# Optimization experiments

Measured on AMD Instinct MI355X. Metric: run time of the kernel, lower is better.

The kernel has to match this reference:

```python
import jax, jax.numpy as jnp
import numpy as np

N_NODES = 4096
N_EDGES = 131072
NUM_USERS = 50000
NUM_ITEMS = 50000
EMB = 64
NUM_CLASSES = 41476
BN_EPS = 1e-5


def _seg_sum(x, idx, n):
    return jax.ops.segment_sum(x, idx, num_segments=n)


def gcn_conv(x, ei, W, b):
    # PyG GCNConv: linear, add self-loops, sym norm D^-1/2 (A+I) D^-1/2, sum-agg, +bias
    n = x.shape[0]
    h = x @ W
    loop = jnp.arange(n, dtype=ei.dtype)
    row = jnp.concatenate([ei[0], loop])
    col = jnp.concatenate([ei[1], loop])
    deg = _seg_sum(jnp.ones_like(col, h.dtype), col, n)
    dinv = jnp.where(deg > 0, deg ** -0.5, 0.0)
    norm = dinv[row] * dinv[col]
    return _seg_sum(h[row] * norm[:, None], col, n) + b


def sage_conv(x, ei, Wl, bl, Wr):
    # PyG SAGEConv (mean aggr): mean_neighbors(x) @ Wl + bl + x @ Wr
    n = x.shape[0]
    ones = jnp.ones((ei.shape[1],), x.dtype)
    cnt = _seg_sum(ones, ei[1], n)
    agg = _seg_sum(x[ei[0]], ei[1], n) / jnp.maximum(cnt, 1.0)[:, None]
    return agg @ Wl + bl + x @ Wr


def cheb_conv(x, ei, W0, W1, b):
    # PyG ChebConv K=2, sym norm, lambda_max=2: L_hat = L - I = -D^-1/2 A D^-1/2
    # out = x @ W0 + (L_hat x) @ W1 + b
    n = x.shape[0]
    ones = jnp.ones((ei.shape[1],), x.dtype)
    deg = _seg_sum(ones, ei[0], n)  # row-sum degree (get_laplacian)
    dinv = jnp.where(deg > 0, deg ** -0.5, 0.0)
    w = -(dinv[ei[0]] * dinv[ei[1]])
    tx1 = _seg_sum(x[ei[0]] * w[:, None], ei[1], n)
    return x @ W0 + tx1 @ W1 + b


def gat_conv(x, ei, W, a_src, a_dst, b):
    # PyG GATConv heads=1, concat=False, self-loops added, leaky_relu(0.2) + softmax over in-edges
    n = x.shape[0]
    h = x @ W
    loop = jnp.arange(n, dtype=ei.dtype)
    row = jnp.concatenate([ei[0], loop])
    col = jnp.concatenate([ei[1], loop])
    a_s = h @ a_src  # [n]
    a_d = h @ a_dst
    e = jax.nn.leaky_relu(a_s[row] + a_d[col], 0.2)
    emax = jax.ops.segment_max(e, col, num_segments=n)  # every segment nonempty (self-loops)
    ex = jnp.exp(e - emax[col])
    denom = _seg_sum(ex, col, n)
    alpha = ex / denom[col]
    return _seg_sum(h[row] * alpha[:, None], col, n) + b


def batch_norm(x, g, be):
    mu = jnp.mean(x, axis=0)
    var = jnp.var(x, axis=0)
    return (x - mu) * jax.lax.rsqrt(var + BN_EPS) * g + be


def setup_inputs() -> dict:
    key = jax.random.key(0)
    ks = iter(jax.random.split(key, 48))
    nrm = lambda shape, s=0.05: jax.random.normal(next(ks), shape, jnp.float32) * s
    edge_index = jax.random.randint(next(ks), (2, N_EDGES), 0, N_NODES, jnp.int32)
    node_x = jax.random.randint(next(ks), (N_NODES, 2), 0, NUM_USERS, jnp.int32)
    inp = dict(
        edge_index=edge_index, node_x=node_x,
        user_emb_w=nrm((NUM_USERS, EMB)), item_emb_w=nrm((NUM_ITEMS, EMB)),
        mlp_w1=nrm((2 * EMB, 1024)), mlp_b1=jnp.zeros((1024,), jnp.float32),
        mlp_w2=nrm((1024, 512)), mlp_b2=jnp.zeros((512,), jnp.float32),
        gcn_w1=nrm((512, 256)), gcn_b1=jnp.zeros((256,), jnp.float32),
        bn1_g=jnp.ones((256,), jnp.float32), bn1_b=jnp.zeros((256,), jnp.float32),
        gcn_w2=nrm((256, 128)), gcn_b2=jnp.zeros((128,), jnp.float32),
        bn2_g=jnp.ones((128,), jnp.float32), bn2_b=jnp.zeros((128,), jnp.float32),
        sage_wl=nrm((128, 128)), sage_bl=jnp.zeros((128,), jnp.float32), sage_wr=nrm((128, 128)),
        cheb_w0=nrm((128, 128)), cheb_w1=nrm((128, 128)), cheb_b=jnp.zeros((128,), jnp.float32),
        gat1_w=nrm((128, 128)), gat1_asrc=nrm((128,)), gat1_adst=nrm((128,)), gat1_b=jnp.zeros((128,), jnp.float32),
        gat2_w=nrm((128, 128)), gat2_asrc=nrm((128,)), gat2_adst=nrm((128,)), gat2_b=jnp.zeros((128,), jnp.float32),
        pred_w=nrm((128, NUM_CLASSES)), pred_b=jnp.zeros((NUM_CLASSES,), jnp.float32),
    )
    return inp


def reference(edge_index, node_x, user_emb_w, item_emb_w, mlp_w1, mlp_b1, mlp_w2, mlp_b2,
              gcn_w1, gcn_b1, bn1_g, bn1_b, gcn_w2, gcn_b2, bn2_g, bn2_b,
              sage_wl, sage_bl, sage_wr, cheb_w0, cheb_w1, cheb_b,
              gat1_w, gat1_asrc, gat1_adst, gat1_b, gat2_w, gat2_asrc, gat2_adst, gat2_b,
              pred_w, pred_b):
    u = user_emb_w[node_x[:, 0]]
    i = item_emb_w[node_x[:, 1]]
    x = jnp.concatenate([u, i], axis=1)  # [N, 2*EMB]
    x = jax.nn.relu(x @ mlp_w1 + mlp_b1)  # dropout = identity (eval mode)
    x = jax.nn.relu(x @ mlp_w2 + mlp_b2)
    x = jax.nn.relu(batch_norm(gcn_conv(x, edge_index, gcn_w1, gcn_b1), bn1_g, bn1_b))
    x = jax.nn.relu(batch_norm(gcn_conv(x, edge_index, gcn_w2, gcn_b2), bn2_g, bn2_b))
    x = jax.nn.relu(sage_conv(x, edge_index, sage_wl, sage_bl, sage_wr))
    x = jax.nn.relu(cheb_conv(x, edge_index, cheb_w0, cheb_w1, cheb_b))
    x = jax.nn.elu(gat_conv(x, edge_index, gat1_w, gat1_asrc, gat1_adst, gat1_b))
    x = jax.nn.elu(gat_conv(x, edge_index, gat2_w, gat2_asrc, gat2_adst, gat2_b))
    return x @ pred_w + pred_b  # [N, NUM_CLASSES]
```

## Files before the change

kernel.cpp:

```cpp
#include <hip/hip_runtime.h>
#include <math.h>

#define NN 4096
#define NE 131072
#define NCLS 41476
#define NPAD 41600

typedef __attribute__((ext_vector_type(8))) unsigned short ushort8;
typedef __attribute__((ext_vector_type(8))) __bf16 bf16x8;
typedef __attribute__((ext_vector_type(4))) float f32x4;

__device__ __forceinline__ unsigned short f2bf(float f) {
  unsigned u = __float_as_uint(f);
  unsigned r = u + 0x7fffu + ((u >> 16) & 1u);
  return (unsigned short)(r >> 16);
}
__device__ __forceinline__ float bf2f(unsigned short u) {
  return __uint_as_float(((unsigned)u) << 16);
}

__global__ void k_gather(const int* __restrict__ node_x, const float* __restrict__ uw,
                         const float* __restrict__ iw, unsigned short* __restrict__ x0) {
  int n = blockIdx.x, t = threadIdx.x;
  int u = node_x[n * 2], it = node_x[n * 2 + 1];
  float v = (t < 64) ? uw[u * 64 + t] : iw[it * 64 + (t - 64)];
  x0[n * 128 + t] = f2bf(v);
}

struct CvtDesc { const float* src; unsigned short* dst; int K, N, ld, koff, tile0, ntx; };
struct CvtArgs { CvtDesc d[11]; };

__global__ void k_cvt_all(CvtArgs a) {
  __shared__ float s[32][33];
  int b = blockIdx.x;
  int di = 0;
#pragma unroll
  for (int i = 1; i < 11; i++)
    if (a.d[i].tile0 <= b) di = i;
  const CvtDesc dd = a.d[di];
  int t = b - dd.tile0;
  int n0 = (t % dd.ntx) * 32, k0 = (t / dd.ntx) * 32;
  int tt = threadIdx.x, c = tt & 31, r8 = tt >> 5;
#pragma unroll
  for (int r = 0; r < 4; r++) {
    int k = k0 + r8 + r * 8, n = n0 + c;
    s[r8 + r * 8][c] = (n < dd.N) ? dd.src[(size_t)k * dd.N + n] : 0.f;
  }
  __syncthreads();
#pragma unroll
  for (int r = 0; r < 4; r++) {
    int n = n0 + r8 + r * 8, k = k0 + c;
    dd.dst[(size_t)n * dd.ld + dd.koff + k] = f2bf(s[c][r8 + r * 8]);
  }
}

template <int OUTBF>
__global__ __launch_bounds__(256) void k_bgemm(const unsigned short* __restrict__ A,
                                               const unsigned short* __restrict__ Bt,
                                               const float* __restrict__ bias,
                                               void* __restrict__ Cv, int N, int K, int relu) {
  __shared__ unsigned short As[128 * 128];
  __shared__ unsigned short Bs[128 * 128];
  int m0 = blockIdx.y * 128;
  int n0 = blockIdx.x * 128;
  int tid = threadIdx.x;
  int wave = tid >> 6, lane = tid & 63;
  int wm = (wave >> 1) * 64, wn = (wave & 1) * 64;
  int lr = lane & 15, lg = lane >> 4;
  f32x4 acc[4][4] = {};
  for (int k0 = 0; k0 < K; k0 += 128) {
#pragma unroll
    for (int i = 0; i < 8; i++) {
      int idx = tid + i * 256;
      int row = idx >> 4, ku = idx & 15;
      int sw = (ku ^ (row & 7)) * 8;
      *reinterpret_cast<ushort8*>(As + row * 128 + sw) =
          *reinterpret_cast<const ushort8*>(A + (size_t)(m0 + row) * K + k0 + ku * 8);
      *reinterpret_cast<ushort8*>(Bs + row * 128 + sw) =
          *reinterpret_cast<const ushort8*>(Bt + (size_t)(n0 + row) * K + k0 + ku * 8);
    }
    __syncthreads();
#pragma unroll
    for (int kk = 0; kk < 4; kk++) {
      bf16x8 af[4], bfr[4];
#pragma unroll
      for (int mi = 0; mi < 4; mi++) {
        int row = wm + mi * 16 + lr;
        af[mi] = __builtin_bit_cast(
            bf16x8, *reinterpret_cast<const ushort8*>(As + row * 128 + (((kk * 4 + lg) ^ (row & 7)) * 8)));
        int col = wn + mi * 16 + lr;
        bfr[mi] = __builtin_bit_cast(
            bf16x8, *reinterpret_cast<const ushort8*>(Bs + col * 128 + (((kk * 4 + lg) ^ (col & 7)) * 8)));
      }
#pragma unroll
      for (int mi = 0; mi < 4; mi++)
#pragma unroll
        for (int ni = 0; ni < 4; ni++)
          acc[mi][ni] = __builtin_amdgcn_mfma_f32_16x16x32_bf16(af[mi], bfr[ni], acc[mi][ni], 0, 0, 0);
    }
    __syncthreads();
  }
#pragma unroll
  for (int mi = 0; mi < 4; mi++) {
#pragma unroll
    for (int ni = 0; ni < 4; ni++) {
      int col = n0 + wn + ni * 16 + lr;
      if (col < N) {
        float bv = bias ? bias[col] : 0.f;
#pragma unroll
        for (int r = 0; r < 4; r++) {
          int row = m0 + wm + mi * 16 + lg * 4 + r;
          float v = acc[mi][ni][r] + bv;
          if (relu) v = fmaxf(v, 0.f);
          if (OUTBF)
            ((unsigned short*)Cv)[(size_t)row * N + col] = f2bf(v);
          else
            ((float*)Cv)[(size_t)row * N + col] = v;
        }
      }
    }
  }
}

__global__ __launch_bounds__(256) void k_bgemm_s(const unsigned short* __restrict__ A,
                                                 const unsigned short* __restrict__ Bt,
                                                 const float* __restrict__ bias,
                                                 unsigned short* __restrict__ C, int ldC,
                                                 int K, int relu) {
  __shared__ unsigned short As[32 * 64];
  __shared__ unsigned short Bs[128 * 64];
  int m0 = blockIdx.y * 32;
  int n0 = blockIdx.x * 128;
  int tid = threadIdx.x;
  int wave = tid >> 6, lane = tid & 63;
  int wn = wave * 32;
  int lr = lane & 15, lg = lane >> 4;
  f32x4 acc[2][2] = {};
  for (int k0 = 0; k0 < K; k0 += 64) {
    {
      int row = tid >> 3, u = tid & 7, sw = (u ^ (row & 7)) * 8;
      *reinterpret_cast<ushort8*>(As + row * 64 + sw) =
          *reinterpret_cast<const ushort8*>(A + (size_t)(m0 + row) * K + k0 + u * 8);
    }
#pragma unroll
    for (int i = 0; i < 4; i++) {
      int idx = tid + i * 256;
      int row = idx >> 3, u = idx & 7, sw = (u ^ (row & 7)) * 8;
      *reinterpret_cast<ushort8*>(Bs + row * 64 + sw) =
          *reinterpret_cast<const ushort8*>(Bt + (size_t)(n0 + row) * K + k0 + u * 8);
    }
    __syncthreads();
#pragma unroll
    for (int kk = 0; kk < 2; kk++) {
      bf16x8 af[2], bfr[2];
#pragma unroll
      for (int mi = 0; mi < 2; mi++) {
        int row = mi * 16 + lr;
        af[mi] = __builtin_bit_cast(
            bf16x8, *reinterpret_cast<const ushort8*>(As + row * 64 + (((kk * 4 + lg) ^ (row & 7)) * 8)));
        int col = wn + mi * 16 + lr;
        bfr[mi] = __builtin_bit_cast(
            bf16x8, *reinterpret_cast<const ushort8*>(Bs + col * 64 + (((kk * 4 + lg) ^ (col & 7)) * 8)));
      }
#pragma unroll
      for (int mi = 0; mi < 2; mi++)
#pragma unroll
        for (int ni = 0; ni < 2; ni++)
          acc[mi][ni] = __builtin_amdgcn_mfma_f32_16x16x32_bf16(af[mi], bfr[ni], acc[mi][ni], 0, 0, 0);
    }
    __syncthreads();
  }
#pragma unroll
  for (int mi = 0; mi < 2; mi++) {
#pragma unroll
    for (int ni = 0; ni < 2; ni++) {
      int col = n0 + wn + ni * 16 + lr;
      float bv = bias ? bias[col] : 0.f;
#pragma unroll
      for (int r = 0; r < 4; r++) {
        int row = m0 + mi * 16 + lg * 4 + r;
        float v = acc[mi][ni][r] + bv;
        if (relu) v = fmaxf(v, 0.f);
        C[(size_t)row * ldC + col] = f2bf(v);
      }
    }
  }
}

__global__ void k_count2(const int* __restrict__ ei, int* __restrict__ deg0,
                         int* __restrict__ deg1) {
  for (int i = blockIdx.x * blockDim.x + threadIdx.x; i < 2 * NE; i += gridDim.x * blockDim.x) {
    int v = ei[i];
    atomicAdd((i < NE ? deg0 : deg1) + v, 1);
  }
}

__global__ void k_dinv(const int* __restrict__ deg, float* __restrict__ dinv, int n, int self) {
  int i = blockIdx.x * blockDim.x + threadIdx.x;
  if (i < n) {
    int d = deg[i] + self;
    dinv[i] = d > 0 ? rsqrtf((float)d) : 0.f;
  }
}

__global__ void k_scan4096(const int* __restrict__ deg, int* __restrict__ rowptr,
                           int* __restrict__ cursor, float* __restrict__ dinvA) {
  __shared__ int s[1024];
  int t = threadIdx.x;
  int4 d = *reinterpret_cast<const int4*>(deg + t * 4);
  float4 dv;
  dv.x = rsqrtf((float)(d.x + 1));
  dv.y = rsqrtf((float)(d.y + 1));
  dv.z = rsqrtf((float)(d.z + 1));
  dv.w = rsqrtf((float)(d.w + 1));
  *reinterpret_cast<float4*>(dinvA + t * 4) = dv;
  int sum = d.x + d.y + d.z + d.w;
  s[t] = sum;
  __syncthreads();
  for (int off = 1; off < 1024; off <<= 1) {
    int x = (t >= off) ? s[t - off] : 0;
    __syncthreads();
    s[t] += x;
    __syncthreads();
  }
  int base = s[t] - sum;
  int4 o;
  o.x = base; o.y = base + d.x; o.z = o.y + d.y; o.w = o.z + d.z;
  *reinterpret_cast<int4*>(rowptr + t * 4) = o;
  *reinterpret_cast<int4*>(cursor + t * 4) = o;
  if (t == 1023) rowptr[4096] = base + sum;
}

__global__ void k_fill(const int* __restrict__ ei0, const int* __restrict__ ei1,
                       int* __restrict__ cursor, int* __restrict__ csr_src) {
  int e = blockIdx.x * blockDim.x + threadIdx.x;
  if (e < NE) {
    int pos = atomicAdd(&cursor[ei1[e]], 1);
    csr_src[pos] = ei0[e];
  }
}

template <int LOGF>
__global__ void k_gcn_agg(const unsigned short* __restrict__ h, const int* __restrict__ rowptr,
                          const int* __restrict__ csr_src, const float* __restrict__ dinv,
                          float* __restrict__ out) {
  __shared__ int sld[128];
  __shared__ float wld[128];
  int c = blockIdx.x, f = threadIdx.x;
  float dc = dinv[c];
  int r0 = rowptr[c], r1 = rowptr[c + 1];
  float acc = bf2f(h[((size_t)c << LOGF) + f]) * dc;
  for (int base = r0; base < r1; base += 128) {
    int nb = min(128, r1 - base);
    if (f < nb) {
      int s = csr_src[base + f];
      sld[f] = s;
      wld[f] = dinv[s];
    }
    __syncthreads();
    for (int i = 0; i < nb; i++) acc += bf2f(h[((size_t)sld[i] << LOGF) + f]) * wld[i];
    __syncthreads();
  }
  out[((size_t)c << LOGF) + f] = acc * dc;
}

__global__ void k_sage_agg(const unsigned short* __restrict__ x, const int* __restrict__ rowptr,
                           const int* __restrict__ csr_src, unsigned short* __restrict__ out) {
  __shared__ int sld[128];
  int c = blockIdx.x, f = threadIdx.x;
  int r0 = rowptr[c], r1 = rowptr[c + 1];
  float acc = 0.f;
  for (int base = r0; base < r1; base += 128) {
    int nb = min(128, r1 - base);
    if (f < nb) sld[f] = csr_src[base + f];
    __syncthreads();
    for (int i = 0; i < nb; i++) acc += bf2f(x[(size_t)sld[i] * 256 + f]);
    __syncthreads();
  }
  out[(size_t)c * 256 + f] = f2bf(acc / fmaxf((float)(r1 - r0), 1.f));
}

__global__ void k_cheb_agg(const unsigned short* __restrict__ x, const int* __restrict__ rowptr,
                           const int* __restrict__ csr_src, const float* __restrict__ dinv0,
                           unsigned short* __restrict__ out) {
  __shared__ int sld[128];
  __shared__ float wld[128];
  int c = blockIdx.x, f = threadIdx.x;
  int r0 = rowptr[c], r1 = rowptr[c + 1];
  float acc = 0.f;
  for (int base = r0; base < r1; base += 128) {
    int nb = min(128, r1 - base);
    if (f < nb) {
      int s = csr_src[base + f];
      sld[f] = s;
      wld[f] = dinv0[s];
    }
    __syncthreads();
    for (int i = 0; i < nb; i++) acc += bf2f(x[(size_t)sld[i] * 256 + f]) * wld[i];
    __syncthreads();
  }
  out[(size_t)c * 256 + f] = f2bf(-acc * dinv0[c]);
}

__global__ void k_gat_agg(const unsigned short* __restrict__ h, const int* __restrict__ rowptr,
                          const int* __restrict__ csr_src, const float* __restrict__ a_s,
                          const float* __restrict__ a_d, const float* __restrict__ bias,
                          unsigned short* __restrict__ out) {
  __shared__ int sld[128];
  __shared__ float eld[128];
  int c = blockIdx.x, f = threadIdx.x;
  int r0 = rowptr[c], r1 = rowptr[c + 1];
  float adc = a_d[c];
  float es = a_s[c] + adc;
  es = es >= 0.f ? es : 0.2f * es;
  float m = es;
  for (int base = r0; base < r1; base += 128) {
    int nb = min(128, r1 - base);
    if (f < nb) {
      float v = a_s[csr_src[base + f]] + adc;
      eld[f] = v >= 0.f ? v : 0.2f * v;
    }
    __syncthreads();
    for (int i = 0; i < nb; i++) m = fmaxf(m, eld[i]);
    __syncthreads();
  }
  float den = expf(es - m);
  float acc = den * bf2f(h[((size_t)c << 7) + f]);
  for (int base = r0; base < r1; base += 128) {
    int nb = min(128, r1 - base);
    if (f < nb) {
      int s = csr_src[base + f];
      sld[f] = s;
      float v = a_s[s] + adc;
      v = v >= 0.f ? v : 0.2f * v;
      eld[f] = expf(v - m);
    }
    __syncthreads();
    for (int i = 0; i < nb; i++) {
      float w = eld[i];
      acc += w * bf2f(h[((size_t)sld[i] << 7) + f]);
      den += w;
    }
    __syncthreads();
  }
  float v = acc / den + bias[f];
  out[((size_t)c << 7) + f] = f2bf(v > 0.f ? v : expm1f(v));
}

__global__ void k_bn_stats(const float* __restrict__ x, float* __restrict__ psum,
                           float* __restrict__ psq, int F) {
  int tid = threadIdx.x;
  int f = tid & (F - 1);
  int rstep = 256 / F;
  int r0 = tid / F;
  int base = blockIdx.x * 64;
  float s = 0.f, s2 = 0.f;
  for (int rr = r0; rr < 64; rr += rstep) {
    float v = x[(size_t)(base + rr) * F + f];
    s += v;
    s2 += v * v;
  }
  int slot = blockIdx.x * rstep + r0;
  psum[(size_t)slot * F + f] = s;
  psq[(size_t)slot * F + f] = s2;
}

__global__ void k_bn_final(const float* __restrict__ psum, const float* __restrict__ psq,
                           const float* __restrict__ g, const float* __restrict__ be,
                           float* __restrict__ scale, float* __restrict__ shift, int F) {
  int f = threadIdx.x;
  int S = 16384 / F;
  float s = 0.f, s2 = 0.f;
  for (int i = 0; i < S; i++) {
    s += psum[(size_t)i * F + f];
    s2 += psq[(size_t)i * F + f];
  }
  float invM = 1.f / (float)NN;
  float mu = s * invM;
  float var = s2 * invM - mu * mu;
  float sc = g[f] * rsqrtf(var + 1e-5f);
  scale[f] = sc;
  shift[f] = be[f] - mu * sc;
}

__global__ void k_bn_apply(const float* __restrict__ x, const float* __restrict__ scale,
                           const float* __restrict__ shift, unsigned short* __restrict__ y,
                           int ldY, int logF, int n) {
  int F1 = (1 << logF) - 1;
  for (int i = blockIdx.x * blockDim.x + threadIdx.x; i < n; i += gridDim.x * blockDim.x) {
    int row = i >> logF, f = i & F1;
    float v = fmaxf(x[i] * scale[f] + shift[f], 0.f);
    y[(size_t)row * ldY + f] = f2bf(v);
  }
}

__global__ void k_gat_dots(const unsigned short* __restrict__ h, const float* __restrict__ asrc,
                           const float* __restrict__ adst, float* __restrict__ a_s,
                           float* __restrict__ a_d) {
  int n = blockIdx.x * 4 + (threadIdx.x >> 6), l = threadIdx.x & 63;
  float h0 = bf2f(h[n * 128 + l]), h1 = bf2f(h[n * 128 + 64 + l]);
  float hs = h0 * asrc[l] + h1 * asrc[64 + l];
  float hd = h0 * adst[l] + h1 * adst[64 + l];
  for (int off = 32; off; off >>= 1) {
    hs += __shfl_down(hs, off, 64);
    hd += __shfl_down(hd, off, 64);
  }
  if (l == 0) {
    a_s[n] = hs;
    a_d[n] = hd;
  }
}

static inline int cdiv(int a, int b) { return (a + b - 1) / b; }

extern "C" void kernel_launch(void* const* d_in, const int* in_sizes, int n_in,
                              void* d_out, int out_size, void* d_ws, size_t ws_size,
                              hipStream_t stream) {
  const int* ei = (const int*)d_in[0];
  const int* ei0 = ei;
  const int* ei1 = ei + NE;
  const int* node_x = (const int*)d_in[1];
  const float* user_w = (const float*)d_in[2];
  const float* item_w = (const float*)d_in[3];
  const float* mlp_w1 = (const float*)d_in[4];
  const float* mlp_b1 = (const float*)d_in[5];
  const float* mlp_w2 = (const float*)d_in[6];
  const float* mlp_b2 = (const float*)d_in[7];
  const float* gcn_w1 = (const float*)d_in[8];
  const float* bn1_g = (const float*)d_in[10];
  const float* bn1_b = (const float*)d_in[11];
  const float* gcn_w2 = (const float*)d_in[12];
  const float* bn2_g = (const float*)d_in[14];
  const float* bn2_b = (const float*)d_in[15];
  const float* sage_wl = (const float*)d_in[16];
  const float* sage_bl = (const float*)d_in[17];
  const float* sage_wr = (const float*)d_in[18];
  const float* cheb_w0 = (const float*)d_in[19];
  const float* cheb_w1 = (const float*)d_in[20];
  const float* cheb_b = (const float*)d_in[21];
  const float* gat1_w = (const float*)d_in[22];
  const float* gat1_as = (const float*)d_in[23];
  const float* gat1_ad = (const float*)d_in[24];
  const float* gat1_b = (const float*)d_in[25];
  const float* gat2_w = (const float*)d_in[26];
  const float* gat2_as = (const float*)d_in[27];
  const float* gat2_ad = (const float*)d_in[28];
  const float* gat2_b = (const float*)d_in[29];
  const float* pred_w = (const float*)d_in[30];
  const float* pred_b = (const float*)d_in[31];

  char* w = (char*)d_ws;
  size_t off = 0;
  auto alloc = [&](size_t bytes) -> char* {
    char* p = w + off;
    off = (off + bytes + 255) & ~(size_t)255;
    return p;
  };
  unsigned short* x0b = (unsigned short*)alloc((size_t)NN * 128 * 2);
  unsigned short* x1b = (unsigned short*)alloc((size_t)NN * 1024 * 2);
  unsigned short* x2b = (unsigned short*)alloc((size_t)NN * 512 * 2);
  unsigned short* h1b = (unsigned short*)alloc((size_t)NN * 256 * 2);
  unsigned short* xab = (unsigned short*)alloc((size_t)NN * 256 * 2);
  unsigned short* catS = (unsigned short*)alloc((size_t)NN * 256 * 2);
  unsigned short* catC = (unsigned short*)alloc((size_t)NN * 256 * 2);
  unsigned short* xb2 = (unsigned short*)alloc((size_t)NN * 128 * 2);
  unsigned short* hb = (unsigned short*)alloc((size_t)NN * 128 * 2);
  unsigned short* xa2 = (unsigned short*)alloc((size_t)NN * 128 * 2);
  unsigned short* xb3 = (unsigned short*)alloc((size_t)NN * 128 * 2);
  float* agg = (float*)alloc((size_t)NN * 256 * 4);
  unsigned short* w1t = (unsigned short*)alloc((size_t)1024 * 128 * 2);
  unsigned short* w2t = (unsigned short*)alloc((size_t)512 * 1024 * 2);
  unsigned short* g1t = (unsigned short*)alloc((size_t)256 * 512 * 2);
  unsigned short* g2t = (unsigned short*)alloc((size_t)128 * 256 * 2);
  unsigned short* sgt = (unsigned short*)alloc((size_t)128 * 256 * 2);
  unsigned short* cht = (unsigned short*)alloc((size_t)128 * 256 * 2);
  unsigned short* a1t = (unsigned short*)alloc((size_t)128 * 128 * 2);
  unsigned short* a2t = (unsigned short*)alloc((size_t)128 * 128 * 2);
  unsigned short* predT = (unsigned short*)alloc((size_t)NPAD * 128 * 2);
  int* deg0 = (int*)alloc(NN * 4);
  int* deg1 = (int*)alloc(NN * 4);
  int* rowptr = (int*)alloc((NN + 1) * 4);
  int* cursor = (int*)alloc(NN * 4);
  int* csr_src = (int*)alloc(NE * 4);
  float* dinvA = (float*)alloc(NN * 4);
  float* dinv0 = (float*)alloc(NN * 4);
  float* a_s = (float*)alloc(NN * 4);
  float* a_d = (float*)alloc(NN * 4);
  float* psum = (float*)alloc(16384 * 4);
  float* psq = (float*)alloc(16384 * 4);
  float* bscale = (float*)alloc(256 * 4);
  float* bshift = (float*)alloc(256 * 4);

  CvtArgs ca;
  int t0 = 0;
  auto mkd = [&](int i, const float* src, unsigned short* dst, int K, int N, int ld, int koff,
                 int ntx) {
    ca.d[i] = {src, dst, K, N, ld, koff, t0, ntx};
    t0 += ntx * (K / 32);
  };
  mkd(0, mlp_w1, w1t, 128, 1024, 128, 0, 32);
  mkd(1, mlp_w2, w2t, 1024, 512, 1024, 0, 16);
  mkd(2, gcn_w1, g1t, 512, 256, 512, 0, 8);
  mkd(3, gcn_w2, g2t, 256, 128, 256, 0, 4);
  mkd(4, sage_wl, sgt, 128, 128, 256, 0, 4);
  mkd(5, sage_wr, sgt, 128, 128, 256, 128, 4);
  mkd(6, cheb_w0, cht, 128, 128, 256, 0, 4);
  mkd(7, cheb_w1, cht, 128, 128, 256, 128, 4);
  mkd(8, gat1_w, a1t, 128, 128, 128, 0, 4);
  mkd(9, gat2_w, a2t, 128, 128, 128, 0, 4);
  mkd(10, pred_w, predT, 128, NCLS, 128, 0, NPAD / 32);
  k_cvt_all<<<t0, 256, 0, stream>>>(ca);

  hipMemsetAsync(deg0, 0, 2 * NN * 4, stream);
  k_count2<<<512, 256, 0, stream>>>(ei, deg0, deg1);
  k_scan4096<<<1, 1024, 0, stream>>>(deg1, rowptr, cursor, dinvA);
  k_fill<<<cdiv(NE, 256), 256, 0, stream>>>(ei0, ei1, cursor, csr_src);
  k_dinv<<<cdiv(NN, 256), 256, 0, stream>>>(deg0, dinv0, NN, 0);

  k_gather<<<NN, 128, 0, stream>>>(node_x, user_w, item_w, x0b);
  k_bgemm<1><<<dim3(8, 32), 256, 0, stream>>>(x0b, w1t, mlp_b1, x1b, 1024, 128, 1);
  k_bgemm<1><<<dim3(4, 32), 256, 0, stream>>>(x1b, w2t, mlp_b2, x2b, 512, 1024, 1);

  k_bgemm_s<<<dim3(2, 128), 256, 0, stream>>>(x2b, g1t, nullptr, h1b, 256, 512, 0);
  k_gcn_agg<8><<<NN, 256, 0, stream>>>(h1b, rowptr, csr_src, dinvA, agg);
  k_bn_stats<<<64, 256, 0, stream>>>(agg, psum, psq, 256);
  k_bn_final<<<1, 256, 0, stream>>>(psum, psq, bn1_g, bn1_b, bscale, bshift, 256);
  k_bn_apply<<<1024, 256, 0, stream>>>(agg, bscale, bshift, xab, 256, 8, NN * 256);

  k_bgemm_s<<<dim3(1, 128), 256, 0, stream>>>(xab, g2t, nullptr, hb, 128, 256, 0);
  k_gcn_agg<7><<<NN, 128, 0, stream>>>(hb, rowptr, csr_src, dinvA, agg);
  k_bn_stats<<<64, 256, 0, stream>>>(agg, psum, psq, 128);
  k_bn_final<<<1, 128, 0, stream>>>(psum, psq, bn2_g, bn2_b, bscale, bshift, 128);
  k_bn_apply<<<1024, 256, 0, stream>>>(agg, bscale, bshift, catS + 128, 256, 7, NN * 128);

  k_sage_agg<<<NN, 128, 0, stream>>>(catS + 128, rowptr, csr_src, catS);
  k_bgemm_s<<<dim3(1, 128), 256, 0, stream>>>(catS, sgt, sage_bl, catC, 256, 256, 1);

  k_cheb_agg<<<NN, 128, 0, stream>>>(catC, rowptr, csr_src, dinv0, catC + 128);
  k_bgemm_s<<<dim3(1, 128), 256, 0, stream>>>(catC, cht, cheb_b, xb2, 128, 256, 1);

  k_bgemm_s<<<dim3(1, 128), 256, 0, stream>>>(xb2, a1t, nullptr, hb, 128, 128, 0);
  k_gat_dots<<<NN / 4, 256, 0, stream>>>(hb, gat1_as, gat1_ad, a_s, a_d);
  k_gat_agg<<<NN, 128, 0, stream>>>(hb, rowptr, csr_src, a_s, a_d, gat1_b, xa2);

  k_bgemm_s<<<dim3(1, 128), 256, 0, stream>>>(xa2, a2t, nullptr, hb, 128, 128, 0);
  k_gat_dots<<<NN / 4, 256, 0, stream>>>(hb, gat2_as, gat2_ad, a_s, a_d);
  k_gat_agg<<<NN, 128, 0, stream>>>(hb, rowptr, csr_src, a_s, a_d, gat2_b, xb3);

  k_bgemm<0><<<dim3(NPAD / 128, 32), 256, 0, stream>>>(xb3, predT, pred_b, (float*)d_out, NCLS, 128, 0);
}
```

Baseline: 510.0 us.

## Fuse BN-apply and GAT dots into GEMMs, stage GEMM epilogue via LDS, widen aggregation

```diff
diff --git a/kernel.cpp b/kernel.cpp
--- a/kernel.cpp
+++ b/kernel.cpp
@@ -59,8 +59,10 @@
                                                const unsigned short* __restrict__ Bt,
                                                const float* __restrict__ bias,
                                                void* __restrict__ Cv, int N, int K, int relu) {
-  __shared__ unsigned short As[128 * 128];
-  __shared__ unsigned short Bs[128 * 128];
+  __shared__ union SU {
+    struct { unsigned short As[128 * 128]; unsigned short Bs[128 * 128]; } s;
+    float Ls[128 * 132];
+  } u;
   int m0 = blockIdx.y * 128;
   int n0 = blockIdx.x * 128;
   int tid = threadIdx.x;
@@ -74,9 +76,9 @@
       int idx = tid + i * 256;
       int row = idx >> 4, ku = idx & 15;
       int sw = (ku ^ (row & 7)) * 8;
-      *reinterpret_cast<ushort8*>(As + row * 128 + sw) =
+      *reinterpret_cast<ushort8*>(u.s.As + row * 128 + sw) =
           *reinterpret_cast<const ushort8*>(A + (size_t)(m0 + row) * K + k0 + ku * 8);
-      *reinterpret_cast<ushort8*>(Bs + row * 128 + sw) =
+      *reinterpret_cast<ushort8*>(u.s.Bs + row * 128 + sw) =
           *reinterpret_cast<const ushort8*>(Bt + (size_t)(n0 + row) * K + k0 + ku * 8);
     }
     __syncthreads();
@@ -87,10 +89,10 @@
       for (int mi = 0; mi < 4; mi++) {
         int row = wm + mi * 16 + lr;
         af[mi] = __builtin_bit_cast(
-            bf16x8, *reinterpret_cast<const ushort8*>(As + row * 128 + (((kk * 4 + lg) ^ (row & 7)) * 8)));
+            bf16x8, *reinterpret_cast<const ushort8*>(u.s.As + row * 128 + (((kk * 4 + lg) ^ (row & 7)) * 8)));
         int col = wn + mi * 16 + lr;
         bfr[mi] = __builtin_bit_cast(
-            bf16x8, *reinterpret_cast<const ushort8*>(Bs + col * 128 + (((kk * 4 + lg) ^ (col & 7)) * 8)));
+            bf16x8, *reinterpret_cast<const ushort8*>(u.s.Bs + col * 128 + (((kk * 4 + lg) ^ (col & 7)) * 8)));
       }
 #pragma unroll
       for (int mi = 0; mi < 4; mi++)
@@ -101,53 +103,109 @@
     __syncthreads();
   }
 #pragma unroll
-  for (int mi = 0; mi < 4; mi++) {
+  for (int mi = 0; mi < 4; mi++)
 #pragma unroll
     for (int ni = 0; ni < 4; ni++) {
-      int col = n0 + wn + ni * 16 + lr;
-      if (col < N) {
-        float bv = bias ? bias[col] : 0.f;
-#pragma unroll
-        for (int r = 0; r < 4; r++) {
-          int row = m0 + wm + mi * 16 + lg * 4 + r;
-          float v = acc[mi][ni][r] + bv;
-          if (relu) v = fmaxf(v, 0.f);
-          if (OUTBF)
-            ((unsigned short*)Cv)[(size_t)row * N + col] = f2bf(v);
-          else
-            ((float*)Cv)[(size_t)row * N + col] = v;
-        }
-      }
-    }
-  }
-}
-
-__global__ __launch_bounds__(256) void k_bgemm_s(const unsigned short* __restrict__ A,
+      int cl = wn + ni * 16 + lr;
+#pragma unroll
+      for (int r = 0; r < 4; r++) {
+        int rl = wm + mi * 16 + lg * 4 + r;
+        u.Ls[rl * 132 + cl] = acc[mi][ni][r];
+      }
+    }
+  __syncthreads();
+  float* Cf = (float*)Cv;
+  unsigned short* Cb = (unsigned short*)Cv;
+#pragma unroll
+  for (int it = 0; it < 8; it++) {
+    int idx = tid + it * 256;
+    int rl = idx >> 4, cb = (idx & 15) * 8;
+    float vv[8];
+    *reinterpret_cast<float4*>(&vv[0]) = *reinterpret_cast<float4*>(&u.Ls[rl * 132 + cb]);
+    *reinterpret_cast<float4*>(&vv[4]) = *reinterpret_cast<float4*>(&u.Ls[rl * 132 + cb + 4]);
+    int col = n0 + cb;
+    size_t row = m0 + rl;
+    if (OUTBF) {
+      float4 b0 = *reinterpret_cast<const float4*>(bias + col);
+      float4 b1 = *reinterpret_cast<const float4*>(bias + col + 4);
+      float bb[8] = {b0.x, b0.y, b0.z, b0.w, b1.x, b1.y, b1.z, b1.w};
+      ushort8 ov;
+#pragma unroll
+      for (int j = 0; j < 8; j++) {
+        float v = vv[j] + bb[j];
+        if (relu) v = fmaxf(v, 0.f);
+        ov[j] = f2bf(v);
+      }
+      *reinterpret_cast<ushort8*>(Cb + row * N + col) = ov;
+    } else {
+      if (col + 8 <= N) {
+        float4 b0 = *reinterpret_cast<const float4*>(bias + col);
+        float4 b1 = *reinterpret_cast<const float4*>(bias + col + 4);
+        float4 o0 = {vv[0] + b0.x, vv[1] + b0.y, vv[2] + b0.z, vv[3] + b0.w};
+        float4 o1 = {vv[4] + b1.x, vv[5] + b1.y, vv[6] + b1.z, vv[7] + b1.w};
+        *reinterpret_cast<float4*>(Cf + row * N + col) = o0;
+        *reinterpret_cast<float4*>(Cf + row * N + col + 4) = o1;
+      } else {
+#pragma unroll
+        for (int j = 0; j < 8; j++)
+          if (col + j < N) Cf[row * N + col + j] = vv[j] + bias[col + j];
+      }
+    }
+  }
+}
+
+template <int MODE>
+__global__ __launch_bounds__(256) void k_bgemm_s(const void* __restrict__ Av,
                                                  const unsigned short* __restrict__ Bt,
                                                  const float* __restrict__ bias,
                                                  unsigned short* __restrict__ C, int ldC,
-                                                 int K, int relu) {
+                                                 int K, int relu,
+                                                 const float* __restrict__ scale,
+                                                 const float* __restrict__ shift,
+                                                 const float* __restrict__ asrc,
+                                                 const float* __restrict__ adst,
+                                                 float* __restrict__ o_as,
+                                                 float* __restrict__ o_ad) {
   __shared__ unsigned short As[32 * 64];
   __shared__ unsigned short Bs[128 * 64];
+  __shared__ float sc[256], sh[256];
+  __shared__ float sas[4][32], sad[4][32];
   int m0 = blockIdx.y * 32;
   int n0 = blockIdx.x * 128;
   int tid = threadIdx.x;
   int wave = tid >> 6, lane = tid & 63;
   int wn = wave * 32;
   int lr = lane & 15, lg = lane >> 4;
+  if (MODE == 1) {
+    if (tid < K) { sc[tid] = scale[tid]; sh[tid] = shift[tid]; }
+    __syncthreads();
+  }
   f32x4 acc[2][2] = {};
   for (int k0 = 0; k0 < K; k0 += 64) {
     {
-      int row = tid >> 3, u = tid & 7, sw = (u ^ (row & 7)) * 8;
-      *reinterpret_cast<ushort8*>(As + row * 64 + sw) =
-          *reinterpret_cast<const ushort8*>(A + (size_t)(m0 + row) * K + k0 + u * 8);
+      int row = tid >> 3, uu = tid & 7, sw = (uu ^ (row & 7)) * 8;
+      if (MODE == 1) {
+        const float* Af = (const float*)Av;
+        const float* p = Af + (size_t)(m0 + row) * K + k0 + uu * 8;
+        float4 p0 = *reinterpret_cast<const float4*>(p);
+        float4 p1 = *reinterpret_cast<const float4*>(p + 4);
+        int kb = k0 + uu * 8;
+        float pv[8] = {p0.x, p0.y, p0.z, p0.w, p1.x, p1.y, p1.z, p1.w};
+        ushort8 o;
+#pragma unroll
+        for (int j = 0; j < 8; j++) o[j] = f2bf(fmaxf(pv[j] * sc[kb + j] + sh[kb + j], 0.f));
+        *reinterpret_cast<ushort8*>(As + row * 64 + sw) = o;
+      } else {
+        *reinterpret_cast<ushort8*>(As + row * 64 + sw) =
+            *reinterpret_cast<const ushort8*>((const unsigned short*)Av + (size_t)(m0 + row) * K + k0 + uu * 8);
+      }
     }
 #pragma unroll
     for (int i = 0; i < 4; i++) {
       int idx = tid + i * 256;
-      int row = idx >> 3, u = idx & 7, sw = (u ^ (row & 7)) * 8;
+      int row = idx >> 3, uu = idx & 7, sw = (uu ^ (row & 7)) * 8;
       *reinterpret_cast<ushort8*>(Bs + row * 64 + sw) =
-          *reinterpret_cast<const ushort8*>(Bt + (size_t)(n0 + row) * K + k0 + u * 8);
+          *reinterpret_cast<const ushort8*>(Bt + (size_t)(n0 + row) * K + k0 + uu * 8);
     }
     __syncthreads();
 #pragma unroll
@@ -170,19 +228,47 @@
     }
     __syncthreads();
   }
+  float dss[2][4] = {}, dsd[2][4] = {};
 #pragma unroll
   for (int mi = 0; mi < 2; mi++) {
 #pragma unroll
     for (int ni = 0; ni < 2; ni++) {
       int col = n0 + wn + ni * 16 + lr;
       float bv = bias ? bias[col] : 0.f;
+      float ac = (MODE == 2) ? asrc[col] : 0.f;
+      float dc = (MODE == 2) ? adst[col] : 0.f;
 #pragma unroll
       for (int r = 0; r < 4; r++) {
         int row = m0 + mi * 16 + lg * 4 + r;
         float v = acc[mi][ni][r] + bv;
         if (relu) v = fmaxf(v, 0.f);
         C[(size_t)row * ldC + col] = f2bf(v);
-      }
+        if (MODE == 2) { dss[mi][r] += v * ac; dsd[mi][r] += v * dc; }
+      }
+    }
+  }
+  if (MODE == 2) {
+#pragma unroll
+    for (int mi = 0; mi < 2; mi++)
+#pragma unroll
+      for (int r = 0; r < 4; r++) {
+#pragma unroll
+        for (int mask = 1; mask < 16; mask <<= 1) {
+          dss[mi][r] += __shfl_xor(dss[mi][r], mask);
+          dsd[mi][r] += __shfl_xor(dsd[mi][r], mask);
+        }
+        if (lr == 0) {
+          int rowloc = mi * 16 + lg * 4 + r;
+          sas[wave][rowloc] = dss[mi][r];
+          sad[wave][rowloc] = dsd[mi][r];
+        }
+      }
+    __syncthreads();
+    if (tid < 32) {
+      float s = sas[0][tid] + sas[1][tid] + sas[2][tid] + sas[3][tid];
+      float d = sad[0][tid] + sad[1][tid] + sad[2][tid] + sad[3][tid];
+      o_as[m0 + tid] = s;
+      o_ad[m0 + tid] = d;
     }
   }
 }
@@ -195,25 +281,19 @@
   }
 }
 
-__global__ void k_dinv(const int* __restrict__ deg, float* __restrict__ dinv, int n, int self) {
-  int i = blockIdx.x * blockDim.x + threadIdx.x;
-  if (i < n) {
-    int d = deg[i] + self;
-    dinv[i] = d > 0 ? rsqrtf((float)d) : 0.f;
-  }
-}
-
-__global__ void k_scan4096(const int* __restrict__ deg, int* __restrict__ rowptr,
-                           int* __restrict__ cursor, float* __restrict__ dinvA) {
+__global__ void k_scan4096(const int* __restrict__ deg1, const int* __restrict__ deg0,
+                           int* __restrict__ rowptr, int* __restrict__ cursor,
+                           float* __restrict__ dinvA, float* __restrict__ dinv0) {
   __shared__ int s[1024];
   int t = threadIdx.x;
-  int4 d = *reinterpret_cast<const int4*>(deg + t * 4);
-  float4 dv;
-  dv.x = rsqrtf((float)(d.x + 1));
-  dv.y = rsqrtf((float)(d.y + 1));
-  dv.z = rsqrtf((float)(d.z + 1));
-  dv.w = rsqrtf((float)(d.w + 1));
+  int4 d = *reinterpret_cast<const int4*>(deg1 + t * 4);
+  float4 dv = {rsqrtf((float)(d.x + 1)), rsqrtf((float)(d.y + 1)),
+               rsqrtf((float)(d.z + 1)), rsqrtf((float)(d.w + 1))};
   *reinterpret_cast<float4*>(dinvA + t * 4) = dv;
+  int4 d0 = *reinterpret_cast<const int4*>(deg0 + t * 4);
+  float4 dv0 = {d0.x > 0 ? rsqrtf((float)d0.x) : 0.f, d0.y > 0 ? rsqrtf((float)d0.y) : 0.f,
+                d0.z > 0 ? rsqrtf((float)d0.z) : 0.f, d0.w > 0 ? rsqrtf((float)d0.w) : 0.f};
+  *reinterpret_cast<float4*>(dinv0 + t * 4) = dv0;
   int sum = d.x + d.y + d.z + d.w;
   s[t] = sum;
   __syncthreads();
@@ -240,44 +320,78 @@
   }
 }
 
-template <int LOGF>
+template <int VEC>
 __global__ void k_gcn_agg(const unsigned short* __restrict__ h, const int* __restrict__ rowptr,
                           const int* __restrict__ csr_src, const float* __restrict__ dinv,
                           float* __restrict__ out) {
+  constexpr int F = 64 * VEC;
   __shared__ int sld[128];
   __shared__ float wld[128];
-  int c = blockIdx.x, f = threadIdx.x;
+  __shared__ float red[3][64 * VEC];
+  int c = blockIdx.x, tid = threadIdx.x, wv = tid >> 6, ln = tid & 63;
   float dc = dinv[c];
   int r0 = rowptr[c], r1 = rowptr[c + 1];
-  float acc = bf2f(h[((size_t)c << LOGF) + f]) * dc;
+  float acc[VEC] = {};
   for (int base = r0; base < r1; base += 128) {
     int nb = min(128, r1 - base);
-    if (f < nb) {
-      int s = csr_src[base + f];
-      sld[f] = s;
-      wld[f] = dinv[s];
-    }
-    __syncthreads();
-    for (int i = 0; i < nb; i++) acc += bf2f(h[((size_t)sld[i] << LOGF) + f]) * wld[i];
-    __syncthreads();
-  }
-  out[((size_t)c << LOGF) + f] = acc * dc;
+    __syncthreads();
+    if (tid < nb) { int s = csr_src[base + tid]; sld[tid] = s; wld[tid] = dinv[s]; }
+    __syncthreads();
+    for (int i = wv; i < nb; i += 4) {
+      float w = wld[i];
+      const unsigned short* p = h + (size_t)sld[i] * F + ln * VEC;
+      if (VEC == 2) {
+        ushort2 v = *reinterpret_cast<const ushort2*>(p);
+        acc[0] += bf2f(v.x) * w; acc[1] += bf2f(v.y) * w;
+      } else {
+        ushort4 v = *reinterpret_cast<const ushort4*>(p);
+        acc[0] += bf2f(v.x) * w; acc[1] += bf2f(v.y) * w;
+        acc[2] += bf2f(v.z) * w; acc[3] += bf2f(v.w) * w;
+      }
+    }
+  }
+  if (wv) {
+#pragma unroll
+    for (int j = 0; j < VEC; j++) red[wv - 1][ln * VEC + j] = acc[j];
+  }
+  __syncthreads();
+  if (wv == 0) {
+    const unsigned short* pc = h + (size_t)c * F + ln * VEC;
+#pragma unroll
+    for (int j = 0; j < VEC; j++) {
+      acc[j] += red[0][ln * VEC + j] + red[1][ln * VEC + j] + red[2][ln * VEC + j];
+      acc[j] += bf2f(pc[j]) * dc;
+      out[(size_t)c * F + ln * VEC + j] = acc[j] * dc;
+    }
+  }
 }
 
 __global__ void k_sage_agg(const unsigned short* __restrict__ x, const int* __restrict__ rowptr,
                            const int* __restrict__ csr_src, unsigned short* __restrict__ out) {
   __shared__ int sld[128];
-  int c = blockIdx.x, f = threadIdx.x;
+  __shared__ float red[3][128];
+  int c = blockIdx.x, tid = threadIdx.x, wv = tid >> 6, ln = tid & 63;
   int r0 = rowptr[c], r1 = rowptr[c + 1];
-  float acc = 0.f;
+  float a0 = 0.f, a1 = 0.f;
   for (int base = r0; base < r1; base += 128) {
     int nb = min(128, r1 - base);
-    if (f < nb) sld[f] = csr_src[base + f];
-    __syncthreads();
-    for (int i = 0; i < nb; i++) acc += bf2f(x[(size_t)sld[i] * 256 + f]);
-    __syncthreads();
-  }
-  out[(size_t)c * 256 + f] = f2bf(acc / fmaxf((float)(r1 - r0), 1.f));
+    __syncthreads();
+    if (tid < nb) sld[tid] = csr_src[base + tid];
+    __syncthreads();
+    for (int i = wv; i < nb; i += 4) {
+      ushort2 v = *reinterpret_cast<const ushort2*>(x + (size_t)sld[i] * 256 + ln * 2);
+      a0 += bf2f(v.x); a1 += bf2f(v.y);
+    }
+  }
+  if (wv) { red[wv - 1][ln * 2] = a0; red[wv - 1][ln * 2 + 1] = a1; }
+  __syncthreads();
+  if (wv == 0) {
+    a0 += red[0][ln * 2] + red[1][ln * 2] + red[2][ln * 2];
+    a1 += red[0][ln * 2 + 1] + red[1][ln * 2 + 1] + red[2][ln * 2 + 1];
+    float inv = 1.f / fmaxf((float)(r1 - r0), 1.f);
+    ushort2 o; o.x = f2bf(a0 * inv); o.y = f2bf(a1 * inv);
+    *reinterpret_cast<ushort2*>(out + (size_t)c * 256 + ln * 2) = o;
+  }
 }
 
 __global__ void k_cheb_agg(const unsigned short* __restrict__ x, const int* __restrict__ rowptr,
@@ -285,21 +399,30 @@
                            unsigned short* __restrict__ out) {
   __shared__ int sld[128];
   __shared__ float wld[128];
-  int c = blockIdx.x, f = threadIdx.x;
+  __shared__ float red[3][128];
+  int c = blockIdx.x, tid = threadIdx.x, wv = tid >> 6, ln = tid & 63;
   int r0 = rowptr[c], r1 = rowptr[c + 1];
-  float acc = 0.f;
+  float a0 = 0.f, a1 = 0.f;
   for (int base = r0; base < r1; base += 128) {
     int nb = min(128, r1 - base);
-    if (f < nb) {
-      int s = csr_src[base + f];
-      sld[f] = s;
-      wld[f] = dinv0[s];
-    }
-    __syncthreads();
-    for (int i = 0; i < nb; i++) acc += bf2f(x[(size_t)sld[i] * 256 + f]) * wld[i];
-    __syncthreads();
-  }
-  out[(size_t)c * 256 + f] = f2bf(-acc * dinv0[c]);
+    __syncthreads();
+    if (tid < nb) { int s = csr_src[base + tid]; sld[tid] = s; wld[tid] = dinv0[s]; }
+    __syncthreads();
+    for (int i = wv; i < nb; i += 4) {
+      float w = wld[i];
+      ushort2 v = *reinterpret_cast<const ushort2*>(x + (size_t)sld[i] * 256 + ln * 2);
+      a0 += bf2f(v.x) * w; a1 += bf2f(v.y) * w;
+    }
+  }
+  if (wv) { red[wv - 1][ln * 2] = a0; red[wv - 1][ln * 2 + 1] = a1; }
+  __syncthreads();
+  if (wv == 0) {
+    a0 += red[0][ln * 2] + red[1][ln * 2] + red[2][ln * 2];
+    a1 += red[0][ln * 2 + 1] + red[1][ln * 2 + 1] + red[2][ln * 2 + 1];
+    float s = -dinv0[c];
+    ushort2 o; o.x = f2bf(a0 * s); o.y = f2bf(a1 * s);
+    *reinterpret_cast<ushort2*>(out + (size_t)c * 256 + ln * 2) = o;
+  }
 }
 
 __global__ void k_gat_agg(const unsigned short* __restrict__ h, const int* __restrict__ rowptr,
@@ -308,43 +431,66 @@
                           unsigned short* __restrict__ out) {
   __shared__ int sld[128];
   __shared__ float eld[128];
-  int c = blockIdx.x, f = threadIdx.x;
+  __shared__ float red[3][128];
+  __shared__ float sden[4];
+  __shared__ float smax[256];
+  int c = blockIdx.x, tid = threadIdx.x, wv = tid >> 6, ln = tid & 63;
   int r0 = rowptr[c], r1 = rowptr[c + 1];
   float adc = a_d[c];
   float es = a_s[c] + adc;
   es = es >= 0.f ? es : 0.2f * es;
   float m = es;
+  for (int i = r0 + tid; i < r1; i += 256) {
+    float v = a_s[csr_src[i]] + adc;
+    m = fmaxf(m, v >= 0.f ? v : 0.2f * v);
+  }
+  smax[tid] = m;
+  __syncthreads();
+  for (int sft = 128; sft; sft >>= 1) {
+    if (tid < sft) smax[tid] = fmaxf(smax[tid], smax[tid + sft]);
+    __syncthreads();
+  }
+  m = smax[0];
+  float a0 = 0.f, a1 = 0.f, den = 0.f;
   for (int base = r0; base < r1; base += 128) {
     int nb = min(128, r1 - base);
-    if (f < nb) {
-      float v = a_s[csr_src[base + f]] + adc;
-      eld[f] = v >= 0.f ? v : 0.2f * v;
-    }
-    __syncthreads();
-    for (int i = 0; i < nb; i++) m = fmaxf(m, eld[i]);
-    __syncthreads();
-  }
-  float den = expf(es - m);
-  float acc = den * bf2f(h[((size_t)c << 7) + f]);
-  for (int base = r0; base < r1; base += 128) {
-    int nb = min(128, r1 - base);
-    if (f < nb) {
-      int s = csr_src[base + f];
-      sld[f] = s;
+    __syncthreads();
+    if (tid < nb) {
+      int s = csr_src[base + tid];
+      sld[tid] = s;
       float v = a_s[s] + adc;
       v = v >= 0.f ? v : 0.2f * v;
-      eld[f] = expf(v - m);
-    }
-    __syncthreads();
-    for (int i = 0; i < nb; i++) {
+      eld[tid] = expf(v - m);
+    }
+    __syncthreads();
+    for (int i = wv; i < nb; i += 4) {
       float w = eld[i];
-      acc += w * bf2f(h[((size_t)sld[i] << 7) + f]);
       den += w;
-    }
-    __syncthreads();
-  }
-  float v = acc / den + bias[f];
-  out[((size_t)c << 7) + f] = f2bf(v > 0.f ? v : expm1f(v));
+      ushort2 v = *reinterpret_cast<const ushort2*>(h + (size_t)sld[i] * 128 + ln * 2);
+      a0 += w * bf2f(v.x); a1 += w * bf2f(v.y);
+    }
+  }
+  if (wv) {
+    red[wv - 1][ln * 2] = a0; red[wv - 1][ln * 2 + 1] = a1;
+    if (ln == 0) sden[wv] = den;
+  }
+  __syncthreads();
+  if (wv == 0) {
+    a0 += red[0][ln * 2] + red[1][ln * 2] + red[2][ln * 2];
+    a1 += red[0][ln * 2 + 1] + red[1][ln * 2 + 1] + red[2][ln * 2 + 1];
+    den += sden[1] + sden[2] + sden[3];
+    float ws = expf(es - m);
+    den += ws;
+    ushort2 xc = *reinterpret_cast<const ushort2*>(h + (size_t)c * 128 + ln * 2);
+    a0 += ws * bf2f(xc.x); a1 += ws * bf2f(xc.y);
+    float inv = 1.f / den;
+    float v0 = a0 * inv + bias[ln * 2];
+    float v1 = a1 * inv + bias[ln * 2 + 1];
+    v0 = v0 > 0.f ? v0 : expm1f(v0);
+    v1 = v1 > 0.f ? v1 : expm1f(v1);
+    ushort2 o; o.x = f2bf(v0); o.y = f2bf(v1);
+    *reinterpret_cast<ushort2*>(out + (size_t)c * 128 + ln * 2) = o;
+  }
 }
 
 __global__ void k_bn_stats(const float* __restrict__ x, float* __restrict__ psum,
@@ -391,23 +537,6 @@
     int row = i >> logF, f = i & F1;
     float v = fmaxf(x[i] * scale[f] + shift[f], 0.f);
     y[(size_t)row * ldY + f] = f2bf(v);
-  }
-}
-
-__global__ void k_gat_dots(const unsigned short* __restrict__ h, const float* __restrict__ asrc,
-                           const float* __restrict__ adst, float* __restrict__ a_s,
-                           float* __restrict__ a_d) {
-  int n = blockIdx.x * 4 + (threadIdx.x >> 6), l = threadIdx.x & 63;
-  float h0 = bf2f(h[n * 128 + l]), h1 = bf2f(h[n * 128 + 64 + l]);
-  float hs = h0 * asrc[l] + h1 * asrc[64 + l];
-  float hd = h0 * adst[l] + h1 * adst[64 + l];
-  for (int off = 32; off; off >>= 1) {
-    hs += __shfl_down(hs, off, 64);
-    hd += __shfl_down(hd, off, 64);
-  }
-  if (l == 0) {
-    a_s[n] = hs;
-    a_d[n] = hd;
   }
 }
 
@@ -460,7 +589,6 @@
   unsigned short* x1b = (unsigned short*)alloc((size_t)NN * 1024 * 2);
   unsigned short* x2b = (unsigned short*)alloc((size_t)NN * 512 * 2);
   unsigned short* h1b = (unsigned short*)alloc((size_t)NN * 256 * 2);
-  unsigned short* xab = (unsigned short*)alloc((size_t)NN * 256 * 2);
   unsigned short* catS = (unsigned short*)alloc((size_t)NN * 256 * 2);
   unsigned short* catC = (unsigned short*)alloc((size_t)NN * 256 * 2);
   unsigned short* xb2 = (unsigned short*)alloc((size_t)NN * 128 * 2);
@@ -513,39 +641,41 @@
 
   hipMemsetAsync(deg0, 0, 2 * NN * 4, stream);
   k_count2<<<512, 256, 0, stream>>>(ei, deg0, deg1);
-  k_scan4096<<<1, 1024, 0, stream>>>(deg1, rowptr, cursor, dinvA);
+  k_scan4096<<<1, 1024, 0, stream>>>(deg1, deg0, rowptr, cursor, dinvA, dinv0);
   k_fill<<<cdiv(NE, 256), 256, 0, stream>>>(ei0, ei1, cursor, csr_src);
-  k_dinv<<<cdiv(NN, 256), 256, 0, stream>>>(deg0, dinv0, NN, 0);
 
   k_gather<<<NN, 128, 0, stream>>>(node_x, user_w, item_w, x0b);
   k_bgemm<1><<<dim3(8, 32), 256, 0, stream>>>(x0b, w1t, mlp_b1, x1b, 1024, 128, 1);
   k_bgemm<1><<<dim3(4, 32), 256, 0, stream>>>(x1b, w2t, mlp_b2, x2b, 512, 1024, 1);
 
-  k_bgemm_s<<<dim3(2, 128), 256, 0, stream>>>(x2b, g1t, nullptr, h1b, 256, 512, 0);
-  k_gcn_agg<8><<<NN, 256, 0, stream>>>(h1b, rowptr, csr_src, dinvA, agg);
+  k_bgemm_s<0><<<dim3(2, 128), 256, 0, stream>>>(x2b, g1t, nullptr, h1b, 256, 512, 0,
+                                                 nullptr, nullptr, nullptr, nullptr, nullptr, nullptr);
+  k_gcn_agg<4><<<NN, 256, 0, stream>>>(h1b, rowptr, csr_src, dinvA, agg);
   k_bn_stats<<<64, 256, 0, stream>>>(agg, psum, psq, 256);
   k_bn_final<<<1, 256, 0, stream>>>(psum, psq, bn1_g, bn1_b, bscale, bshift, 256);
-  k_bn_apply<<<1024, 256, 0, stream>>>(agg, bscale, bshift, xab, 256, 8, NN * 256);
-
-  k_bgemm_s<<<dim3(1, 128), 256, 0, stream>>>(xab, g2t, nullptr, hb, 128, 256, 0);
-  k_gcn_agg<7><<<NN, 128, 0, stream>>>(hb, rowptr, csr_src, dinvA, agg);
+
+  k_bgemm_s<1><<<dim3(1, 128), 256, 0, stream>>>(agg, g2t, nullptr, hb, 128, 256, 0,
+                                                 bscale, bshift, nullptr, nullptr, nullptr, nullptr);
+  k_gcn_agg<2><<<NN, 256, 0, stream>>>(hb, rowptr, csr_src, dinvA, agg);
   k_bn_stats<<<64, 256, 0, stream>>>(agg, psum, psq, 128);
   k_bn_final<<<1, 128, 0, stream>>>(psum, psq, bn2_g, bn2_b, bscale, bshift, 128);
   k_bn_apply<<<1024, 256, 0, stream>>>(agg, bscale, bshift, catS + 128, 256, 7, NN * 128);
 
-  k_sage_agg<<<NN, 128, 0, stream>>>(catS + 128, rowptr, csr_src, catS);
-  k_bgemm_s<<<dim3(1, 128), 256, 0, stream>>>(catS, sgt, sage_bl, catC, 256, 256, 1);
-
-  k_cheb_agg<<<NN, 128, 0, stream>>>(catC, rowptr, csr_src, dinv0, catC + 128);
-  k_bgemm_s<<<dim3(1, 128), 256, 0, stream>>>(catC, cht, cheb_b, xb2, 128, 256, 1);
-
-  k_bgemm_s<<<dim3(1, 128), 256, 0, stream>>>(xb2, a1t, nullptr, hb, 128, 128, 0);
-  k_gat_dots<<<NN / 4, 256, 0, stream>>>(hb, gat1_as, gat1_ad, a_s, a_d);
-  k_gat_agg<<<NN, 128, 0, stream>>>(hb, rowptr, csr_src, a_s, a_d, gat1_b, xa2);
-
-  k_bgemm_s<<<dim3(1, 128), 256, 0, stream>>>(xa2, a2t, nullptr, hb, 128, 128, 0);
-  k_gat_dots<<<NN / 4, 256, 0, stream>>>(hb, gat2_as, gat2_ad, a_s, a_d);
-  k_gat_agg<<<NN, 128, 0, stream>>>(hb, rowptr, csr_src, a_s, a_d, gat2_b, xb3);
+  k_sage_agg<<<NN, 256, 0, stream>>>(catS + 128, rowptr, csr_src, catS);
+  k_bgemm_s<0><<<dim3(1, 128), 256, 0, stream>>>(catS, sgt, sage_bl, catC, 256, 256, 1,
+                                                 nullptr, nullptr, nullptr, nullptr, nullptr, nullptr);
+
+  k_cheb_agg<<<NN, 256, 0, stream>>>(catC, rowptr, csr_src, dinv0, catC + 128);
+  k_bgemm_s<0><<<dim3(1, 128), 256, 0, stream>>>(catC, cht, cheb_b, xb2, 128, 256, 1,
+                                                 nullptr, nullptr, nullptr, nullptr, nullptr, nullptr);
+
+  k_bgemm_s<2><<<dim3(1, 128), 256, 0, stream>>>(xb2, a1t, nullptr, hb, 128, 128, 0,
+                                                 nullptr, nullptr, gat1_as, gat1_ad, a_s, a_d);
+  k_gat_agg<<<NN, 256, 0, stream>>>(hb, rowptr, csr_src, a_s, a_d, gat1_b, xa2);
+
+  k_bgemm_s<2><<<dim3(1, 128), 256, 0, stream>>>(xa2, a2t, nullptr, hb, 128, 128, 0,
+                                                 nullptr, nullptr, gat2_as, gat2_ad, a_s, a_d);
+  k_gat_agg<<<NN, 256, 0, stream>>>(hb, rowptr, csr_src, a_s, a_d, gat2_b, xb3);
 
   k_bgemm<0><<<dim3(NPAD / 128, 32), 256, 0, stream>>>(xb3, predT, pred_b, (float*)d_out, NCLS, 128, 0);
 }
```

New measurement: 666.4 us. 1.31x slower.
